# Performance work log

Measured on AMD Instinct MI355X. Metric: run time of the kernel, lower is better.

## Reference

```python
import jax, jax.numpy as jnp
import numpy as np

B, T, I, H, O = 8192, 1024, 7, 100, 1


def setup_inputs() -> dict:
    key = jax.random.key(0)
    ks = jax.random.split(key, 7)
    s = 1.0 / np.sqrt(H)  # PyTorch default init bound for RNN/Linear(H)
    return {
        "x": jax.random.normal(ks[0], (B, T, I), dtype=jnp.float32),
        "W_ih": jax.random.uniform(ks[1], (H, I), jnp.float32, -s, s),
        "W_hh": jax.random.uniform(ks[2], (H, H), jnp.float32, -s, s),
        "b_ih": jax.random.uniform(ks[3], (H,), jnp.float32, -s, s),
        "b_hh": jax.random.uniform(ks[4], (H,), jnp.float32, -s, s),
        "W_fc": jax.random.uniform(ks[5], (O, H), jnp.float32, -s, s),
        "b_fc": jax.random.uniform(ks[6], (O,), jnp.float32, -s, s),
    }


def reference(x, W_ih, W_hh, b_ih, b_hh, W_fc, b_fc):
    # Precompute the input projection for all timesteps in one GEMM:
    # x_proj[b,t,h] = x[b,t,:] @ W_ih^T + b_ih + b_hh  (both biases folded in)
    x_proj = jnp.einsum('bti,hi->bth', x, W_ih) + b_ih + b_hh  # [B,T,H]

    def step(h, xt):
        # h_t = relu(x_t W_ih^T + b_ih + h_{t-1} W_hh^T + b_hh)
        h_new = jax.nn.relu(xt + h @ W_hh.T)
        return h_new, None

    h0 = jnp.zeros((x.shape[0], W_hh.shape[0]), dtype=x.dtype)  # [B,H]
    hT, _ = jax.lax.scan(step, h0, jnp.swapaxes(x_proj, 0, 1))  # scan over T

    # fc applied to last timestep only: out[:, -1, :] @ W_fc^T + b_fc
    return hT @ W_fc.T + b_fc  # [B,O]
```

## Files before the change

### kernel.cpp

```cpp
#include <hip/hip_runtime.h>


typedef _Float16 half8 __attribute__((ext_vector_type(8)));
typedef float f32x4 __attribute__((ext_vector_type(4)));
typedef unsigned u32x4 __attribute__((ext_vector_type(4)));

static __device__ __forceinline__ unsigned pkrtz(float a, float b) {
    return __builtin_bit_cast(unsigned, __builtin_amdgcn_cvt_pkrtz(a, b));
}

__global__ __launch_bounds__(64, 1)
void rnn_wave(const float* __restrict__ x,
              const float* __restrict__ W_ih,
              const float* __restrict__ W_hh,
              const float* __restrict__ b_ih,
              const float* __restrict__ b_hh,
              const float* __restrict__ W_fc,
              const float* __restrict__ b_fc,
              float* __restrict__ out) {
    const int l  = threadIdx.x;
    const int lm = l & 15;
    const int q  = l >> 4;
    const bool q1   = (q == 1);
    const bool qlt2 = (q < 2);

    half8 w[7][4];
#pragma unroll
    for (int ti = 0; ti < 7; ++ti) {
        const int np = 16 * ti + lm;
#pragma unroll
        for (int kt = 0; kt < 4; ++kt) {
            half8 hw;
#pragma unroll
            for (int jj = 0; jj < 8; ++jj) {
                float v = 0.f;
                if (np < 100) {
                    if (jj < 4) {
                        int p = 16 * kt + 4 * q + jj;
                        if (p < 100) v = W_hh[np * 100 + p];
                    } else if (kt < 3) {
                        int p = 16 * (kt + 4) + 4 * q + (jj - 4);
                        if (p < 100) v = W_hh[np * 100 + p];
                    } else {
                        if (q == 0)      v = W_ih[np * 7 + (jj - 4)];
                        else if (q == 1) v = (jj < 7) ? W_ih[np * 7 + jj]
                                             : (b_ih[np] + b_hh[np]);
                    }
                }
                hw[jj] = (_Float16)v;
            }
            w[ti][kt] = hw;
        }
    }

    const float* xr = x + (size_t)(blockIdx.x * 16 + lm) * 7168;
    const int o0 = q1 ? 4 : 0, o1 = o0 + 1, o2 = o0 + 2, o3 = q1 ? 6 : 3;

    half8 hf[4];
    {
        float v0 = xr[o0], v1 = xr[o1], v2 = xr[o2], v3 = xr[o3];
        u32x4 z = {0u, 0u, 0u, 0u};
        hf[0] = __builtin_bit_cast(half8, z);
        hf[1] = hf[0];
        hf[2] = hf[0];
        unsigned xd0 = pkrtz(v0, v1);
        unsigned xd1 = pkrtz(v2, q1 ? 1.0f : v3);
        if (!qlt2) { xd0 = 0u; xd1 = 0u; }
        u32x4 h3 = {0u, 0u, xd0, xd1};
        hf[3] = __builtin_bit_cast(half8, h3);
    }

    float xv[4][4];
#pragma unroll
    for (int s = 1; s <= 4; ++s) {
        const float* p = xr + s * 7;
        xv[s & 3][0] = p[o0]; xv[s & 3][1] = p[o1];
        xv[s & 3][2] = p[o2]; xv[s & 3][3] = p[o3];
    }

    const f32x4 kZ = {0.f, 0.f, 0.f, 0.f};
    f32x4 acc[7];

    for (int tb = 0; tb < 1024; tb += 4) {
#pragma unroll
        for (int u = 0; u < 4; ++u) {
            const int t = tb + u;

#pragma unroll
            for (int kt = 0; kt < 4; ++kt) {
                const int order[7] = {0, 4, 1, 5, 2, 6, 3};
#pragma unroll
                for (int oi = 0; oi < 7; ++oi) {
                    const int ti = order[oi];
                    acc[ti] = __builtin_amdgcn_mfma_f32_16x16x32_f16(
                        w[ti][kt], hf[kt], (kt == 0) ? kZ : acc[ti], 0, 0, 0);
                }
            }

            const int s = (u + 1) & 3;
#pragma unroll
            for (int kt = 0; kt < 3; ++kt) {
                u32x4 d;
                d.x = pkrtz(fmaxf(acc[kt][0], 0.f),     fmaxf(acc[kt][1], 0.f));
                d.y = pkrtz(fmaxf(acc[kt][2], 0.f),     fmaxf(acc[kt][3], 0.f));
                d.z = pkrtz(fmaxf(acc[kt + 4][0], 0.f), fmaxf(acc[kt + 4][1], 0.f));
                d.w = pkrtz(fmaxf(acc[kt + 4][2], 0.f), fmaxf(acc[kt + 4][3], 0.f));
                hf[kt] = __builtin_bit_cast(half8, d);
            }
            {
                unsigned xd0 = pkrtz(xv[s][0], xv[s][1]);
                unsigned xd1 = pkrtz(xv[s][2], q1 ? 1.0f : xv[s][3]);
                if (!qlt2) { xd0 = 0u; xd1 = 0u; }
                u32x4 d;
                d.x = pkrtz(fmaxf(acc[3][0], 0.f), fmaxf(acc[3][1], 0.f));
                d.y = pkrtz(fmaxf(acc[3][2], 0.f), fmaxf(acc[3][3], 0.f));
                d.z = xd0; d.w = xd1;
                hf[3] = __builtin_bit_cast(half8, d);
            }

            int tn = t + 5; if (tn > 1023) tn = 1023;
            const float* p = xr + tn * 7;
            xv[s][0] = p[o0]; xv[s][1] = p[o1];
            xv[s][2] = p[o2]; xv[s][3] = p[o3];
        }
    }

    float sum = 0.f;
#pragma unroll
    for (int ti = 0; ti < 7; ++ti) {
#pragma unroll
        for (int r = 0; r < 4; ++r) {
            const int np = 16 * ti + 4 * q + r;
            const float wf = (np < 100) ? W_fc[np] : 0.f;
            sum += wf * fmaxf(acc[ti][r], 0.f);
        }
    }
    sum += __shfl_xor(sum, 16, 64);
    sum += __shfl_xor(sum, 32, 64);
    if (q == 0) out[blockIdx.x * 16 + lm] = sum + b_fc[0];
}

extern "C" void kernel_launch(void* const* d_in, const int* in_sizes, int n_in,
                              void* d_out, int out_size, void* d_ws, size_t ws_size,
                              hipStream_t stream) {
    const float* x    = (const float*)d_in[0];
    const float* W_ih = (const float*)d_in[1];
    const float* W_hh = (const float*)d_in[2];
    const float* b_ih = (const float*)d_in[3];
    const float* b_hh = (const float*)d_in[4];
    const float* W_fc = (const float*)d_in[5];
    const float* b_fc = (const float*)d_in[6];
    float* out = (float*)d_out;

    rnn_wave<<<dim3(512), dim3(64), 0, stream>>>(x, W_ih, W_hh, b_ih, b_hh, W_fc, b_fc, out);
}
```

Baseline: 619.7 us.

## Interleave two independent 16-row batch chains per wave to hide MFMA latency

Each wave now processes 32 batch rows as two independent recurrence chains (A and B), interleaving their MFMAs so one chain's dependent accumulation latency overlaps the other's. The grid is halved to 256 blocks, so fewer waves run across the CUs. The ReLU on three of the four hidden fragments is also applied after the fp16 pack, using a packed half max instead of scalar fmaxf. Register pressure roughly doubles for accumulators and hidden state, and with 256 single-wave blocks each CU may hold only one wave, so the serial chain must be hidden by the interleave alone.

```diff
diff --git a/kernel.cpp b/kernel.cpp
--- a/kernel.cpp
+++ b/kernel.cpp
@@ -10,19 +10,22 @@
 }
 
 __global__ __launch_bounds__(64, 1)
-void rnn_wave(const float* __restrict__ x,
-              const float* __restrict__ W_ih,
-              const float* __restrict__ W_hh,
-              const float* __restrict__ b_ih,
-              const float* __restrict__ b_hh,
-              const float* __restrict__ W_fc,
-              const float* __restrict__ b_fc,
-              float* __restrict__ out) {
+void rnn_wave2(const float* __restrict__ x,
+               const float* __restrict__ W_ih,
+               const float* __restrict__ W_hh,
+               const float* __restrict__ b_ih,
+               const float* __restrict__ b_hh,
+               const float* __restrict__ W_fc,
+               const float* __restrict__ b_fc,
+               float* __restrict__ out) {
     const int l  = threadIdx.x;
     const int lm = l & 15;
     const int q  = l >> 4;
     const bool q1   = (q == 1);
     const bool qlt2 = (q < 2);
+
+    const u32x4 zz = {0u, 0u, 0u, 0u};
+    const half8 hzero = __builtin_bit_cast(half8, zz);
 
     half8 w[7][4];
 #pragma unroll
@@ -53,16 +56,17 @@
         }
     }
 
-    const float* xr = x + (size_t)(blockIdx.x * 16 + lm) * 7168;
+    const float* xrA = x + (size_t)(blockIdx.x * 32 + lm) * 7168;
+    const float* xrB = xrA + (size_t)16 * 7168;
     const int o0 = q1 ? 4 : 0, o1 = o0 + 1, o2 = o0 + 2, o3 = q1 ? 6 : 3;
 
-    half8 hf[4];
-    {
+    half8 hfA[4], hfB[4];
+#pragma unroll
+    for (int c = 0; c < 2; ++c) {
+        const float* xr = c ? xrB : xrA;
+        half8* hf = c ? hfB : hfA;
         float v0 = xr[o0], v1 = xr[o1], v2 = xr[o2], v3 = xr[o3];
-        u32x4 z = {0u, 0u, 0u, 0u};
-        hf[0] = __builtin_bit_cast(half8, z);
-        hf[1] = hf[0];
-        hf[2] = hf[0];
+        hf[0] = hzero; hf[1] = hzero; hf[2] = hzero;
         unsigned xd0 = pkrtz(v0, v1);
         unsigned xd1 = pkrtz(v2, q1 ? 1.0f : v3);
         if (!qlt2) { xd0 = 0u; xd1 = 0u; }
@@ -70,16 +74,19 @@
         hf[3] = __builtin_bit_cast(half8, h3);
     }
 
-    float xv[4][4];
+    float xvA[4][4], xvB[4][4];
 #pragma unroll
     for (int s = 1; s <= 4; ++s) {
-        const float* p = xr + s * 7;
-        xv[s & 3][0] = p[o0]; xv[s & 3][1] = p[o1];
-        xv[s & 3][2] = p[o2]; xv[s & 3][3] = p[o3];
+        const float* pA = xrA + s * 7;
+        const float* pB = xrB + s * 7;
+        xvA[s & 3][0] = pA[o0]; xvA[s & 3][1] = pA[o1];
+        xvA[s & 3][2] = pA[o2]; xvA[s & 3][3] = pA[o3];
+        xvB[s & 3][0] = pB[o0]; xvB[s & 3][1] = pB[o1];
+        xvB[s & 3][2] = pB[o2]; xvB[s & 3][3] = pB[o3];
     }
 
     const f32x4 kZ = {0.f, 0.f, 0.f, 0.f};
-    f32x4 acc[7];
+    f32x4 accA[7], accB[7];
 
     for (int tb = 0; tb < 1024; tb += 4) {
 #pragma unroll
@@ -92,52 +99,68 @@
 #pragma unroll
                 for (int oi = 0; oi < 7; ++oi) {
                     const int ti = order[oi];
-                    acc[ti] = __builtin_amdgcn_mfma_f32_16x16x32_f16(
-                        w[ti][kt], hf[kt], (kt == 0) ? kZ : acc[ti], 0, 0, 0);
+                    accA[ti] = __builtin_amdgcn_mfma_f32_16x16x32_f16(
+                        w[ti][kt], hfA[kt], (kt == 0) ? kZ : accA[ti], 0, 0, 0);
+                    accB[ti] = __builtin_amdgcn_mfma_f32_16x16x32_f16(
+                        w[ti][kt], hfB[kt], (kt == 0) ? kZ : accB[ti], 0, 0, 0);
                 }
             }
 
             const int s = (u + 1) & 3;
 #pragma unroll
-            for (int kt = 0; kt < 3; ++kt) {
-                u32x4 d;
-                d.x = pkrtz(fmaxf(acc[kt][0], 0.f),     fmaxf(acc[kt][1], 0.f));
-                d.y = pkrtz(fmaxf(acc[kt][2], 0.f),     fmaxf(acc[kt][3], 0.f));
-                d.z = pkrtz(fmaxf(acc[kt + 4][0], 0.f), fmaxf(acc[kt + 4][1], 0.f));
-                d.w = pkrtz(fmaxf(acc[kt + 4][2], 0.f), fmaxf(acc[kt + 4][3], 0.f));
-                hf[kt] = __builtin_bit_cast(half8, d);
-            }
-            {
-                unsigned xd0 = pkrtz(xv[s][0], xv[s][1]);
-                unsigned xd1 = pkrtz(xv[s][2], q1 ? 1.0f : xv[s][3]);
-                if (!qlt2) { xd0 = 0u; xd1 = 0u; }
-                u32x4 d;
-                d.x = pkrtz(fmaxf(acc[3][0], 0.f), fmaxf(acc[3][1], 0.f));
-                d.y = pkrtz(fmaxf(acc[3][2], 0.f), fmaxf(acc[3][3], 0.f));
-                d.z = xd0; d.w = xd1;
-                hf[3] = __builtin_bit_cast(half8, d);
+            for (int c = 0; c < 2; ++c) {
+                f32x4*  acc = c ? accB : accA;
+                half8*  hf  = c ? hfB  : hfA;
+                float*  xs  = c ? xvB[s] : xvA[s];
+#pragma unroll
+                for (int kt = 0; kt < 3; ++kt) {
+                    u32x4 d;
+                    d.x = pkrtz(acc[kt][0],     acc[kt][1]);
+                    d.y = pkrtz(acc[kt][2],     acc[kt][3]);
+                    d.z = pkrtz(acc[kt + 4][0], acc[kt + 4][1]);
+                    d.w = pkrtz(acc[kt + 4][2], acc[kt + 4][3]);
+                    half8 hv = __builtin_bit_cast(half8, d);
+                    hf[kt] = __builtin_elementwise_max(hv, hzero);
+                }
+                {
+                    unsigned xd0 = pkrtz(xs[0], xs[1]);
+                    unsigned xd1 = pkrtz(xs[2], q1 ? 1.0f : xs[3]);
+                    if (!qlt2) { xd0 = 0u; xd1 = 0u; }
+                    u32x4 d;
+                    d.x = pkrtz(fmaxf(acc[3][0], 0.f), fmaxf(acc[3][1], 0.f));
+                    d.y = pkrtz(fmaxf(acc[3][2], 0.f), fmaxf(acc[3][3], 0.f));
+                    d.z = xd0; d.w = xd1;
+                    hf[3] = __builtin_bit_cast(half8, d);
+                }
             }
 
             int tn = t + 5; if (tn > 1023) tn = 1023;
-            const float* p = xr + tn * 7;
-            xv[s][0] = p[o0]; xv[s][1] = p[o1];
-            xv[s][2] = p[o2]; xv[s][3] = p[o3];
+            const float* pA = xrA + tn * 7;
+            const float* pB = xrB + tn * 7;
+            xvA[s][0] = pA[o0]; xvA[s][1] = pA[o1];
+            xvA[s][2] = pA[o2]; xvA[s][3] = pA[o3];
+            xvB[s][0] = pB[o0]; xvB[s][1] = pB[o1];
+            xvB[s][2] = pB[o2]; xvB[s][3] = pB[o3];
         }
     }
 
-    float sum = 0.f;
 #pragma unroll
-    for (int ti = 0; ti < 7; ++ti) {
+    for (int c = 0; c < 2; ++c) {
+        f32x4* acc = c ? accB : accA;
+        float sum = 0.f;
 #pragma unroll
-        for (int r = 0; r < 4; ++r) {
-            const int np = 16 * ti + 4 * q + r;
-            const float wf = (np < 100) ? W_fc[np] : 0.f;
-            sum += wf * fmaxf(acc[ti][r], 0.f);
+        for (int ti = 0; ti < 7; ++ti) {
+#pragma unroll
+            for (int r = 0; r < 4; ++r) {
+                const int np = 16 * ti + 4 * q + r;
+                const float wf = (np < 100) ? W_fc[np] : 0.f;
+                sum += wf * fmaxf(acc[ti][r], 0.f);
+            }
         }
+        sum += __shfl_xor(sum, 16, 64);
+        sum += __shfl_xor(sum, 32, 64);
+        if (q == 0) out[blockIdx.x * 32 + c * 16 + lm] = sum + b_fc[0];
     }
-    sum += __shfl_xor(sum, 16, 64);
-    sum += __shfl_xor(sum, 32, 64);
-    if (q == 0) out[blockIdx.x * 16 + lm] = sum + b_fc[0];
 }
 
 extern "C" void kernel_launch(void* const* d_in, const int* in_sizes, int n_in,
@@ -152,5 +175,5 @@
     const float* b_fc = (const float*)d_in[6];
     float* out = (float*)d_out;
 
-    rnn_wave<<<dim3(512), dim3(64), 0, stream>>>(x, W_ih, W_hh, b_ih, b_hh, W_fc, b_fc, out);
+    rnn_wave2<<<dim3(256), dim3(64), 0, stream>>>(x, W_ih, W_hh, b_ih, b_hh, W_fc, b_fc, out);
 }
```

New measurement: 1.006 ms. 62.3% more time.

## Interleave MFMA chains with packed-half ReLU and explicit sched barriers per step

Applied to the files above, without the earlier changes.

Reorders each recurrence step so the MFMA chains for tiles 0/1/4/5 finish first and their outputs are packed into the next hidden-state buffer while the remaining tiles' MFMAs are still issuing. Hidden state is double-buffered (hfA/hfB), and ReLU is applied with a packed half8 max after conversion instead of per-float fmax. sched_group_barrier hints interleave VALU and VMEM work with MFMA issue. The aim is to hide the conversion and x-load latency behind matrix work on the serial critical path. The risk is that the hand-written scheduling hints are miscounted or fight the compiler's own schedule.

```diff
diff --git a/kernel.cpp b/kernel.cpp
--- a/kernel.cpp
+++ b/kernel.cpp
@@ -5,12 +5,15 @@
 typedef float f32x4 __attribute__((ext_vector_type(4)));
 typedef unsigned u32x4 __attribute__((ext_vector_type(4)));
 
+#define MF(a, b, c) __builtin_amdgcn_mfma_f32_16x16x32_f16((a), (b), (c), 0, 0, 0)
+#define SGB __builtin_amdgcn_sched_group_barrier
+
 static __device__ __forceinline__ unsigned pkrtz(float a, float b) {
     return __builtin_bit_cast(unsigned, __builtin_amdgcn_cvt_pkrtz(a, b));
 }
 
 __global__ __launch_bounds__(64, 1)
-void rnn_wave(const float* __restrict__ x,
+void rnn_pipe(const float* __restrict__ x,
               const float* __restrict__ W_ih,
               const float* __restrict__ W_hh,
               const float* __restrict__ b_ih,
@@ -21,8 +24,11 @@
     const int l  = threadIdx.x;
     const int lm = l & 15;
     const int q  = l >> 4;
-    const bool q1   = (q == 1);
-    const bool qlt2 = (q < 2);
+    const bool q1 = (q == 1);
+    const unsigned xmask = (q < 2) ? 0xffffffffu : 0u;
+
+    const u32x4 zz = {0u, 0u, 0u, 0u};
+    const half8 hzero = __builtin_bit_cast(half8, zz);
 
     half8 w[7][4];
 #pragma unroll
@@ -56,18 +62,14 @@
     const float* xr = x + (size_t)(blockIdx.x * 16 + lm) * 7168;
     const int o0 = q1 ? 4 : 0, o1 = o0 + 1, o2 = o0 + 2, o3 = q1 ? 6 : 3;
 
-    half8 hf[4];
+    half8 hfA[4], hfB[4];
     {
         float v0 = xr[o0], v1 = xr[o1], v2 = xr[o2], v3 = xr[o3];
-        u32x4 z = {0u, 0u, 0u, 0u};
-        hf[0] = __builtin_bit_cast(half8, z);
-        hf[1] = hf[0];
-        hf[2] = hf[0];
-        unsigned xd0 = pkrtz(v0, v1);
-        unsigned xd1 = pkrtz(v2, q1 ? 1.0f : v3);
-        if (!qlt2) { xd0 = 0u; xd1 = 0u; }
+        hfA[0] = hzero; hfA[1] = hzero; hfA[2] = hzero;
+        unsigned xd0 = pkrtz(v0, v1) & xmask;
+        unsigned xd1 = pkrtz(v2, q1 ? 1.0f : v3) & xmask;
         u32x4 h3 = {0u, 0u, xd0, xd1};
-        hf[3] = __builtin_bit_cast(half8, h3);
+        hfA[3] = __builtin_bit_cast(half8, h3);
     }
 
     float xv[4][4];
@@ -77,52 +79,66 @@
         xv[s & 3][0] = p[o0]; xv[s & 3][1] = p[o1];
         xv[s & 3][2] = p[o2]; xv[s & 3][3] = p[o3];
     }
+    const float* pa = xr + 35 + o0;
+    const float* pb = xr + 35 + o3;
 
     const f32x4 kZ = {0.f, 0.f, 0.f, 0.f};
     f32x4 acc[7];
 
+#define PACKH(HWd, A, Bb)                                                     \
+    { u32x4 d;                                                                \
+      d.x = pkrtz(A[0], A[1]);  d.y = pkrtz(A[2], A[3]);                      \
+      d.z = pkrtz(Bb[0], Bb[1]); d.w = pkrtz(Bb[2], Bb[3]);                   \
+      half8 hv = __builtin_bit_cast(half8, d);                                \
+      HWd = __builtin_elementwise_max(hv, hzero); }
+
+#define STEP(HR, HW, S, T)                                                    \
+    {                     \
+      acc[0] = MF(w[0][0], HR[0], kZ);     acc[4] = MF(w[4][0], HR[0], kZ);   \
+      acc[1] = MF(w[1][0], HR[0], kZ);     acc[5] = MF(w[5][0], HR[0], kZ);   \
+      acc[0] = MF(w[0][1], HR[1], acc[0]); acc[4] = MF(w[4][1], HR[1], acc[4]);\
+      acc[1] = MF(w[1][1], HR[1], acc[1]); acc[5] = MF(w[5][1], HR[1], acc[5]);\
+      acc[0] = MF(w[0][2], HR[2], acc[0]); acc[4] = MF(w[4][2], HR[2], acc[4]);\
+      acc[1] = MF(w[1][2], HR[2], acc[1]); acc[5] = MF(w[5][2], HR[2], acc[5]);\
+      acc[0] = MF(w[0][3], HR[3], acc[0]); acc[4] = MF(w[4][3], HR[3], acc[4]);\
+      acc[1] = MF(w[1][3], HR[3], acc[1]); acc[5] = MF(w[5][3], HR[3], acc[5]);\
+      PACKH(HW[0], acc[0], acc[4]);     \
+                            \
+      acc[2] = MF(w[2][0], HR[0], kZ);     acc[6] = MF(w[6][0], HR[0], kZ);   \
+      acc[3] = MF(w[3][0], HR[0], kZ);                                        \
+      acc[2] = MF(w[2][1], HR[1], acc[2]); acc[6] = MF(w[6][1], HR[1], acc[6]);\
+      acc[3] = MF(w[3][1], HR[1], acc[3]);                                    \
+      acc[2] = MF(w[2][2], HR[2], acc[2]); acc[6] = MF(w[6][2], HR[2], acc[6]);\
+      acc[3] = MF(w[3][2], HR[2], acc[3]);                                    \
+      acc[2] = MF(w[2][3], HR[3], acc[2]); acc[6] = MF(w[6][3], HR[3], acc[6]);\
+      acc[3] = MF(w[3][3], HR[3], acc[3]);                                    \
+      PACKH(HW[1], acc[1], acc[5]);                                           \
+      PACKH(HW[2], acc[2], acc[6]);                                           \
+      { unsigned xd0 = pkrtz(xv[S][0], xv[S][1]) & xmask;                     \
+        unsigned xd1 = pkrtz(xv[S][2], q1 ? 1.0f : xv[S][3]) & xmask;         \
+        u32x4 d;                                                              \
+        d.x = pkrtz(fmaxf(acc[3][0], 0.f), fmaxf(acc[3][1], 0.f));            \
+        d.y = pkrtz(fmaxf(acc[3][2], 0.f), fmaxf(acc[3][3], 0.f));            \
+        d.z = xd0; d.w = xd1;                                                 \
+        HW[3] = __builtin_bit_cast(half8, d); }                               \
+      if ((T) < 1019) {    \
+        xv[S][0] = pa[0]; xv[S][1] = pa[1]; xv[S][2] = pa[2]; xv[S][3] = pb[0];\
+        pa += 7; pb += 7;                                                     \
+      }                                                                       \
+        \
+      SGB(8, 16, 0); SGB(2, 8, 0);                                            \
+      SGB(8, 3, 0);  SGB(2, 4, 0);                                            \
+      SGB(8, 3, 0);  SGB(2, 4, 0);                                            \
+      SGB(8, 3, 0);  SGB(2, 4, 0);                                            \
+      SGB(8, 3, 0);  SGB(2, 4, 0);                                            \
+      SGB(32, 4, 0); SGB(2, 24, 0);                                           \
+    }
+
     for (int tb = 0; tb < 1024; tb += 4) {
-#pragma unroll
-        for (int u = 0; u < 4; ++u) {
-            const int t = tb + u;
-
-#pragma unroll
-            for (int kt = 0; kt < 4; ++kt) {
-                const int order[7] = {0, 4, 1, 5, 2, 6, 3};
-#pragma unroll
-                for (int oi = 0; oi < 7; ++oi) {
-                    const int ti = order[oi];
-                    acc[ti] = __builtin_amdgcn_mfma_f32_16x16x32_f16(
-                        w[ti][kt], hf[kt], (kt == 0) ? kZ : acc[ti], 0, 0, 0);
-                }
-            }
-
-            const int s = (u + 1) & 3;
-#pragma unroll
-            for (int kt = 0; kt < 3; ++kt) {
-                u32x4 d;
-                d.x = pkrtz(fmaxf(acc[kt][0], 0.f),     fmaxf(acc[kt][1], 0.f));
-                d.y = pkrtz(fmaxf(acc[kt][2], 0.f),     fmaxf(acc[kt][3], 0.f));
-                d.z = pkrtz(fmaxf(acc[kt + 4][0], 0.f), fmaxf(acc[kt + 4][1], 0.f));
-                d.w = pkrtz(fmaxf(acc[kt + 4][2], 0.f), fmaxf(acc[kt + 4][3], 0.f));
-                hf[kt] = __builtin_bit_cast(half8, d);
-            }
-            {
-                unsigned xd0 = pkrtz(xv[s][0], xv[s][1]);
-                unsigned xd1 = pkrtz(xv[s][2], q1 ? 1.0f : xv[s][3]);
-                if (!qlt2) { xd0 = 0u; xd1 = 0u; }
-                u32x4 d;
-                d.x = pkrtz(fmaxf(acc[3][0], 0.f), fmaxf(acc[3][1], 0.f));
-                d.y = pkrtz(fmaxf(acc[3][2], 0.f), fmaxf(acc[3][3], 0.f));
-                d.z = xd0; d.w = xd1;
-                hf[3] = __builtin_bit_cast(half8, d);
-            }
-
-            int tn = t + 5; if (tn > 1023) tn = 1023;
-            const float* p = xr + tn * 7;
-            xv[s][0] = p[o0]; xv[s][1] = p[o1];
-            xv[s][2] = p[o2]; xv[s][3] = p[o3];
-        }
+        STEP(hfA, hfB, 1, tb + 0)
+        STEP(hfB, hfA, 2, tb + 1)
+        STEP(hfA, hfB, 3, tb + 2)
+        STEP(hfB, hfA, 0, tb + 3)
     }
 
     float sum = 0.f;
@@ -152,5 +168,5 @@
     const float* b_fc = (const float*)d_in[6];
     float* out = (float*)d_out;
 
-    rnn_wave<<<dim3(512), dim3(64), 0, stream>>>(x, W_ih, W_hh, b_ih, b_hh, W_fc, b_fc, out);
+    rnn_pipe<<<dim3(512), dim3(64), 0, stream>>>(x, W_ih, W_hh, b_ih, b_hh, W_fc, b_fc, out);
 }
```

Result: slower. 658.2 us (+6.2%).
